# Optimization experiments

Hardware: AMD Instinct MI355X
Metric: run time of the kernel (lower is better)

The kernel has to match this reference:

```python
import jax, jax.numpy as jnp
import numpy as np

DIM = 2048
N_HEADS = 16
HEAD_DIM = 128
EPS = 1e-6


def setup_inputs() -> dict:
    key = jax.random.key(0)
    ks = jax.random.split(key, 8)
    b, gf, gh, gw = 1, 8, 16, 24
    s = gf * gh * gw
    c = HEAD_DIM // 2
    w = lambda k: 0.02 * jax.random.normal(k, (DIM, DIM), jnp.float32)
    return {
        "x": jax.random.normal(ks[0], (b, s, DIM), jnp.float32),
        "freqs_angle": jax.random.normal(ks[1], (1024, c), jnp.float32),
        "Wq": w(ks[2]), "bq": jnp.zeros((DIM,), jnp.float32),
        "Wk": w(ks[3]), "bk": jnp.zeros((DIM,), jnp.float32),
        "Wv": w(ks[4]), "bv": jnp.zeros((DIM,), jnp.float32),
        "Wo": w(ks[5]), "bo": jnp.zeros((DIM,), jnp.float32),
        "gq": jnp.ones((DIM,), jnp.float32),
        "gk": jnp.ones((DIM,), jnp.float32),
        "seq_len": s, "grid_f": gf, "grid_h": gh, "grid_w": gw,
    }


def _rms(t, g):
    return t * jax.lax.rsqrt(jnp.mean(t * t, axis=-1, keepdims=True) + EPS) * g


def _grid_angles(freqs_angle, gf, gh, gw, c):
    # band split [c - 2*(c//3), c//3, c//3] as in rope_apply
    cf = c - 2 * (c // 3)
    ch = cw = c // 3
    af = freqs_angle[:gf, :cf]            # [F, cf]
    ah = freqs_angle[:gh, cf:cf + ch]     # [H, ch]
    aw = freqs_angle[:gw, cf + ch:c]      # [W, cw]
    ang = jnp.concatenate([
        jnp.broadcast_to(af[:, None, None, :], (gf, gh, gw, cf)),
        jnp.broadcast_to(ah[None, :, None, :], (gf, gh, gw, ch)),
        jnp.broadcast_to(aw[None, None, :, :], (gf, gh, gw, cw)),
    ], axis=-1)
    return ang.reshape(gf * gh * gw, c)   # [s, c]


def reference(x, freqs_angle, Wq, bq, Wk, bk, Wv, bv, Wo, bo, gq, gk,
              seq_len, grid_f, grid_h, grid_w):
    b, s, _ = x.shape
    n, d = N_HEADS, HEAD_DIM
    c = d // 2
    ang = _grid_angles(freqs_angle, grid_f, grid_h, grid_w, c)
    cos = jnp.cos(ang)[None, :, None, :]  # [1, s, 1, c]
    sin = jnp.sin(ang)[None, :, None, :]

    def rope(t):  # complex multiply on (even, odd) = (real, imag) pairs
        te, to = t[..., 0::2], t[..., 1::2]
        return jnp.stack([te * cos - to * sin, te * sin + to * cos], axis=-1).reshape(t.shape)

    q = _rms(x @ Wq.T + bq, gq).reshape(b, s, n, d)
    k = _rms(x @ Wk.T + bk, gk).reshape(b, s, n, d)
    v = (x @ Wv.T + bv).reshape(b, s, n, d)
    q, k = rope(q), rope(k)

    scale = np.float32(1.0 / np.sqrt(d))
    scores = jnp.einsum('bqnd,bknd->bnqk', q, k) * scale
    p = jax.nn.softmax(scores, axis=-1)
    o = jnp.einsum('bnqk,bknd->bqnd', p, v).reshape(b, s, n * d)
    return o @ Wo.T + bo
```

## Files before the change

### kernel.cpp

```cpp
#include <hip/hip_runtime.h>
#include <stdint.h>
#include <stddef.h>

typedef __bf16 bf16_t;
typedef __bf16 bf16x8 __attribute__((ext_vector_type(8)));
typedef __bf16 bf16x4 __attribute__((ext_vector_type(4)));
typedef __bf16 bf16x2 __attribute__((ext_vector_type(2)));
typedef float  f32x4  __attribute__((ext_vector_type(4)));

#define SEQ   3072
#define DIMD  2048
#define NH    16
#define HD    128
#define QKVN  6144

__device__ __forceinline__ void async16(const bf16_t* g, bf16_t* l) {
  __builtin_amdgcn_global_load_lds((const __attribute__((address_space(1))) uint32_t*)g,
                                   (__attribute__((address_space(3))) uint32_t*)l, 16, 0, 0);
}

__global__ __launch_bounds__(256) void cvt_bf16(const float* __restrict__ in,
                                                bf16_t* __restrict__ out, int n) {
  int idx = (blockIdx.x * 256 + threadIdx.x) * 8;
  if (idx + 7 < n) {
    const float4 a = *(const float4*)(in + idx);
    const float4 b = *(const float4*)(in + idx + 4);
    bf16x8 o;
    o[0] = (bf16_t)a.x; o[1] = (bf16_t)a.y; o[2] = (bf16_t)a.z; o[3] = (bf16_t)a.w;
    o[4] = (bf16_t)b.x; o[5] = (bf16_t)b.y; o[6] = (bf16_t)b.z; o[7] = (bf16_t)b.w;
    *(bf16x8*)(out + idx) = o;
  }
}

__global__ __launch_bounds__(256) void pack_bias(const float* __restrict__ bq,
                                                 const float* __restrict__ bk,
                                                 const float* __restrict__ bv,
                                                 float* __restrict__ bqkv) {
  int t = blockIdx.x * 256 + threadIdx.x;
  float v;
  if (t < 2048)      v = bq[t];
  else if (t < 4096) v = bk[t - 2048];
  else               v = bv[t - 4096];
  bqkv[t] = v;
}

template<bool OUT_BF16>
__global__ __launch_bounds__(256, 2) void gemm_nt(const bf16_t* __restrict__ A,
                                                  const bf16_t* __restrict__ B,
                                                  const float* __restrict__ bias,
                                                  void* __restrict__ Cout,
                                                  int M, int N, int K) {
  __shared__ __align__(16) bf16_t As[128 * 64];
  __shared__ __align__(16) bf16_t Bs[128 * 64];
  const int t = threadIdx.x;
  const int lane = t & 63, wave = t >> 6;
  const int quad = lane >> 4, l15 = lane & 15;
  const int wy = wave >> 1, wx = wave & 1;
  const size_t bm = (size_t)blockIdx.y * 128, bn = (size_t)blockIdx.x * 128;
  const bf16_t* Ab = A + bm * K;
  const bf16_t* Bb = B + bn * K;
  f32x4 acc[4][4] = {};
  int srow[4], scol[4];
#pragma unroll
  for (int r = 0; r < 4; r++) {
    int L = r * 256 + t;
    int row = L >> 3, cp = L & 7;
    srow[r] = row;
    scol[r] = (cp ^ (row & 7)) * 8;
  }
  for (int k0 = 0; k0 < K; k0 += 64) {
    __syncthreads();
#pragma unroll
    for (int r = 0; r < 4; r++)
      async16(Ab + (size_t)srow[r] * K + k0 + scol[r], &As[(r * 256 + t) * 8]);
#pragma unroll
    for (int r = 0; r < 4; r++)
      async16(Bb + (size_t)srow[r] * K + k0 + scol[r], &Bs[(r * 256 + t) * 8]);
    __syncthreads();
#pragma unroll
    for (int ks = 0; ks < 2; ks++) {
      bf16x8 af[4], bfv[4];
#pragma unroll
      for (int i = 0; i < 4; i++) {
        int row = wy * 64 + i * 16 + l15;
        af[i] = *(const bf16x8*)&As[row * 64 + (((ks * 4 + quad) ^ (row & 7)) * 8)];
      }
#pragma unroll
      for (int j = 0; j < 4; j++) {
        int row = wx * 64 + j * 16 + l15;
        bfv[j] = *(const bf16x8*)&Bs[row * 64 + (((ks * 4 + quad) ^ (row & 7)) * 8)];
      }
#pragma unroll
      for (int i = 0; i < 4; i++)
#pragma unroll
        for (int j = 0; j < 4; j++)
          acc[i][j] = __builtin_amdgcn_mfma_f32_16x16x32_bf16(af[i], bfv[j], acc[i][j], 0, 0, 0);
    }
  }
#pragma unroll
  for (int i = 0; i < 4; i++) {
#pragma unroll
    for (int j = 0; j < 4; j++) {
      size_t row = bm + wy * 64 + i * 16 + quad * 4;
      size_t col = bn + wx * 64 + j * 16 + l15;
      float bb = bias[col];
#pragma unroll
      for (int r = 0; r < 4; r++) {
        float v = acc[i][j][r] + bb;
        if (OUT_BF16) ((bf16_t*)Cout)[(row + r) * N + col] = (bf16_t)v;
        else          ((float*)Cout)[(row + r) * N + col] = v;
      }
    }
  }
}

__global__ __launch_bounds__(256) void rmsrope(bf16_t* __restrict__ qkv,
                                               const float* __restrict__ gq,
                                               const float* __restrict__ gk,
                                               const float* __restrict__ freqs) {
  const int s = blockIdx.x, t = threadIdx.x;
  bf16_t* row = qkv + (size_t)s * QKVN;
  bf16x8 qv = *(const bf16x8*)&row[t * 8];
  bf16x8 kv = *(const bf16x8*)&row[2048 + t * 8];
  float qf[8], kf[8];
  float qs = 0.f, ks2 = 0.f;
#pragma unroll
  for (int i = 0; i < 8; i++) {
    qf[i] = (float)qv[i]; qs  += qf[i] * qf[i];
    kf[i] = (float)kv[i]; ks2 += kf[i] * kf[i];
  }
#pragma unroll
  for (int m = 1; m < 64; m <<= 1) {
    qs  += __shfl_xor(qs, m);
    ks2 += __shfl_xor(ks2, m);
  }
  __shared__ float red[2][4];
  const int wave = t >> 6, lane = t & 63;
  if (lane == 0) { red[0][wave] = qs; red[1][wave] = ks2; }
  __syncthreads();
  qs  = red[0][0] + red[0][1] + red[0][2] + red[0][3];
  ks2 = red[1][0] + red[1][1] + red[1][2] + red[1][3];
  const float qsc = rsqrtf(qs  / 2048.f + 1e-6f);
  const float ksc = rsqrtf(ks2 / 2048.f + 1e-6f);
  const int sf = s / 384, rem = s - sf * 384;
  const int sh = rem / 24, sw = rem - sh * 24;
  bf16x8 qo, ko;
#pragma unroll
  for (int u = 0; u < 4; u++) {
    const int col = t * 8 + 2 * u;
    const int i = (col >> 1) & 63;
    const int frow = (i < 22) ? sf : ((i < 43) ? sh : sw);
    const float ang = freqs[frow * 64 + i];
    float sn, cs;
    __sincosf(ang, &sn, &cs);
    float te = qf[2 * u]     * qsc * gq[col];
    float to = qf[2 * u + 1] * qsc * gq[col + 1];
    qo[2 * u]     = (bf16_t)(te * cs - to * sn);
    qo[2 * u + 1] = (bf16_t)(te * sn + to * cs);
    te = kf[2 * u]     * ksc * gk[col];
    to = kf[2 * u + 1] * ksc * gk[col + 1];
    ko[2 * u]     = (bf16_t)(te * cs - to * sn);
    ko[2 * u + 1] = (bf16_t)(te * sn + to * cs);
  }
  *(bf16x8*)&row[t * 8] = qo;
  *(bf16x8*)&row[2048 + t * 8] = ko;
}

__global__ __launch_bounds__(256, 2) void flash_attn(const bf16_t* __restrict__ qkv,
                                                     bf16_t* __restrict__ ob) {
  __shared__ __align__(16) bf16_t Ks[64 * 128];
  __shared__ __align__(16) bf16_t Vt[128 * 64];
  __shared__ __align__(16) bf16_t Ps[4][32 * 64];
  const int h = blockIdx.y, qt = blockIdx.x;
  const int s0 = qt * 128;
  const int t = threadIdx.x, wave = t >> 6, lane = t & 63;
  const int quad = lane >> 4, l15 = lane & 15;
  const int wq = wave * 32;
  const float scale = 0.08838834764831845f;
  bf16x8 qfr[2][4];
#pragma unroll
  for (int tj = 0; tj < 2; tj++)
#pragma unroll
    for (int ks = 0; ks < 4; ks++)
      qfr[tj][ks] = *(const bf16x8*)&qkv[(size_t)(s0 + wq + tj * 16 + l15) * QKVN + h * HD + ks * 32 + quad * 8];
  f32x4 oacc[2][8] = {};
  float m_run[2] = {-3e38f, -3e38f}, l_run[2] = {0.f, 0.f};
  const int pp = t & 31, bb = t >> 5;
  for (int kt = 0; kt < SEQ / 64; kt++) {
    const int kv0 = kt * 64;
    __syncthreads();
#pragma unroll
    for (int r = 0; r < 4; r++) {
      int L = r * 256 + t, krow = L >> 4, cp = L & 15;
      int c = cp ^ (krow & 7);
      async16(qkv + (size_t)(kv0 + krow) * QKVN + 2048 + h * HD + c * 8, &Ks[L * 8]);
    }
#pragma unroll
    for (int s2 = 0; s2 < 2; s2++) {
      const int d0 = (bb + s2 * 8) * 8;
      bf16x8 va = *(const bf16x8*)&qkv[(size_t)(kv0 + 2 * pp)     * QKVN + 4096 + h * HD + d0];
      bf16x8 vb = *(const bf16x8*)&qkv[(size_t)(kv0 + 2 * pp + 1) * QKVN + 4096 + h * HD + d0];
#pragma unroll
      for (int i = 0; i < 8; i++) {
        const int d = d0 + i;
        const int cp2 = (pp >> 2) ^ (d & 7);
        bf16x2 pr; pr[0] = va[i]; pr[1] = vb[i];
        *(bf16x2*)&Vt[d * 64 + cp2 * 8 + (pp & 3) * 2] = pr;
      }
    }
    __syncthreads();
    f32x4 st[4][2] = {};
#pragma unroll
    for (int ks = 0; ks < 4; ks++) {
      bf16x8 kfr[4];
#pragma unroll
      for (int ti = 0; ti < 4; ti++) {
        const int kr = ti * 16 + l15;
        kfr[ti] = *(const bf16x8*)&Ks[kr * 128 + (((ks * 4 + quad) ^ (kr & 7)) * 8)];
      }
#pragma unroll
      for (int ti = 0; ti < 4; ti++)
#pragma unroll
        for (int tj = 0; tj < 2; tj++)
          st[ti][tj] = __builtin_amdgcn_mfma_f32_16x16x32_bf16(kfr[ti], qfr[tj][ks], st[ti][tj], 0, 0, 0);
    }
    float mt[2] = {-3e38f, -3e38f};
#pragma unroll
    for (int ti = 0; ti < 4; ti++)
#pragma unroll
      for (int tj = 0; tj < 2; tj++)
#pragma unroll
        for (int r = 0; r < 4; r++) {
          st[ti][tj][r] *= scale;
          mt[tj] = fmaxf(mt[tj], st[ti][tj][r]);
        }
    float al[2];
#pragma unroll
    for (int tj = 0; tj < 2; tj++) {
      mt[tj] = fmaxf(mt[tj], __shfl_xor(mt[tj], 16));
      mt[tj] = fmaxf(mt[tj], __shfl_xor(mt[tj], 32));
      const float mn = fmaxf(m_run[tj], mt[tj]);
      al[tj] = __expf(m_run[tj] - mn);
      m_run[tj] = mn;
    }
    float lt[2] = {0.f, 0.f};
#pragma unroll
    for (int ti = 0; ti < 4; ti++)
#pragma unroll
      for (int tj = 0; tj < 2; tj++) {
        bf16x4 pv;
#pragma unroll
        for (int r = 0; r < 4; r++) {
          const float p = __expf(st[ti][tj][r] - m_run[tj]);
          pv[r] = (bf16_t)p;
          lt[tj] += (float)pv[r];
        }
        const int q = tj * 16 + l15;
        const int cp2 = (ti * 2 + (quad >> 1)) ^ (q & 7);
        *(bf16x4*)&Ps[wave][q * 64 + cp2 * 8 + (quad & 1) * 4] = pv;
      }
#pragma unroll
    for (int tj = 0; tj < 2; tj++) {
      lt[tj] += __shfl_xor(lt[tj], 16);
      lt[tj] += __shfl_xor(lt[tj], 32);
      l_run[tj] = l_run[tj] * al[tj] + lt[tj];
    }
#pragma unroll
    for (int ti = 0; ti < 2; ti++) {
      float a0 = __shfl(al[ti], quad * 4 + 0);
      float a1 = __shfl(al[ti], quad * 4 + 1);
      float a2 = __shfl(al[ti], quad * 4 + 2);
      float a3 = __shfl(al[ti], quad * 4 + 3);
#pragma unroll
      for (int dj = 0; dj < 8; dj++) {
        oacc[ti][dj][0] *= a0; oacc[ti][dj][1] *= a1;
        oacc[ti][dj][2] *= a2; oacc[ti][dj][3] *= a3;
      }
    }
#pragma unroll
    for (int ks = 0; ks < 2; ks++) {
      bf16x8 pf[2], vf[8];
#pragma unroll
      for (int ti = 0; ti < 2; ti++) {
        const int q = ti * 16 + l15;
        pf[ti] = *(const bf16x8*)&Ps[wave][q * 64 + (((ks * 4 + quad) ^ (q & 7)) * 8)];
      }
#pragma unroll
      for (int dj = 0; dj < 8; dj++) {
        const int d = dj * 16 + l15;
        vf[dj] = *(const bf16x8*)&Vt[d * 64 + (((ks * 4 + quad) ^ (d & 7)) * 8)];
      }
#pragma unroll
      for (int ti = 0; ti < 2; ti++)
#pragma unroll
        for (int dj = 0; dj < 8; dj++)
          oacc[ti][dj] = __builtin_amdgcn_mfma_f32_16x16x32_bf16(pf[ti], vf[dj], oacc[ti][dj], 0, 0, 0);
    }
  }
#pragma unroll
  for (int ti = 0; ti < 2; ti++) {
    float li[4];
#pragma unroll
    for (int r = 0; r < 4; r++) li[r] = 1.f / __shfl(l_run[ti], quad * 4 + r);
#pragma unroll
    for (int dj = 0; dj < 8; dj++)
#pragma unroll
      for (int r = 0; r < 4; r++) {
        const float v = oacc[ti][dj][r] * li[r];
        ob[(size_t)(s0 + wq + ti * 16 + quad * 4 + r) * DIMD + h * HD + dj * 16 + l15] = (bf16_t)v;
      }
  }
}

extern "C" void kernel_launch(void* const* d_in, const int* in_sizes, int n_in,
                              void* d_out, int out_size, void* d_ws, size_t ws_size,
                              hipStream_t stream) {
  (void)in_sizes; (void)n_in; (void)out_size;
  const float* x     = (const float*)d_in[0];
  const float* freqs = (const float*)d_in[1];
  const float* Wq    = (const float*)d_in[2];
  const float* bq    = (const float*)d_in[3];
  const float* Wk    = (const float*)d_in[4];
  const float* bk    = (const float*)d_in[5];
  const float* Wv    = (const float*)d_in[6];
  const float* bv    = (const float*)d_in[7];
  const float* Wo    = (const float*)d_in[8];
  const float* bo    = (const float*)d_in[9];
  const float* gq    = (const float*)d_in[10];
  const float* gk    = (const float*)d_in[11];

  char* w = (char*)d_ws;
  bf16_t* xb    = (bf16_t*)(w);
  bf16_t* Wqkvb = (bf16_t*)(w + 12582912);
  bf16_t* Wob   = (bf16_t*)(w + 37748736);
  bf16_t* qkvb  = (bf16_t*)(w + 46137344);
  bf16_t* obuf  = (bf16_t*)(w + 83886080);
  float*  bqkv  = (float*) (w + 96468992);
  if (ws_size < (size_t)96493568) return;

  cvt_bf16<<<3072, 256, 0, stream>>>(x, xb, 6291456);
  cvt_bf16<<<2048, 256, 0, stream>>>(Wq, Wqkvb, 4194304);
  cvt_bf16<<<2048, 256, 0, stream>>>(Wk, Wqkvb + 4194304, 4194304);
  cvt_bf16<<<2048, 256, 0, stream>>>(Wv, Wqkvb + 8388608, 4194304);
  cvt_bf16<<<2048, 256, 0, stream>>>(Wo, Wob, 4194304);
  pack_bias<<<24, 256, 0, stream>>>(bq, bk, bv, bqkv);

  gemm_nt<true><<<dim3(48, 24), 256, 0, stream>>>(xb, Wqkvb, bqkv, qkvb, SEQ, QKVN, DIMD);
  rmsrope<<<3072, 256, 0, stream>>>(qkvb, gq, gk, freqs);
  flash_attn<<<dim3(24, NH), 256, 0, stream>>>(qkvb, obuf);
  gemm_nt<false><<<dim3(16, 24), 256, 0, stream>>>(obuf, Wob, bo, (float*)d_out, SEQ, DIMD, DIMD);
}
```

Baseline: 472.5 us.

## Split flash attention KV range in halves and merge with log-sum-exp combine

Flash attention now splits the key/value sequence into two halves along a third grid dimension, doubling the block count from 384 to 768 so more of the GPU's compute units are busy. Each half writes a normalized bf16 partial output plus its running max and sum, and a new combine kernel merges them using softmax rescaling. The launch bound is raised to three blocks per CU. In exchange it adds an extra kernel launch, extra global traffic for the partial outputs, and a second bf16 rounding step. The workspace regions holding the converted x and weights are reused for the partials after the QKV GEMM.

After: 544.0 us. +15.1%, slower.

```diff
diff --git a/kernel.cpp b/kernel.cpp
--- a/kernel.cpp
+++ b/kernel.cpp
@@ -166,12 +166,13 @@
   *(bf16x8*)&row[2048 + t * 8] = ko;
 }
 
-__global__ __launch_bounds__(256, 2) void flash_attn(const bf16_t* __restrict__ qkv,
-                                                     bf16_t* __restrict__ ob) {
+__global__ __launch_bounds__(256, 3) void flash_attn(const bf16_t* __restrict__ qkv,
+                                                     bf16_t* __restrict__ opart,
+                                                     float2* __restrict__ ml) {
   __shared__ __align__(16) bf16_t Ks[64 * 128];
   __shared__ __align__(16) bf16_t Vt[128 * 64];
   __shared__ __align__(16) bf16_t Ps[4][32 * 64];
-  const int h = blockIdx.y, qt = blockIdx.x;
+  const int h = blockIdx.y, qt = blockIdx.x, half = blockIdx.z;
   const int s0 = qt * 128;
   const int t = threadIdx.x, wave = t >> 6, lane = t & 63;
   const int quad = lane >> 4, l15 = lane & 15;
@@ -186,8 +187,8 @@
   f32x4 oacc[2][8] = {};
   float m_run[2] = {-3e38f, -3e38f}, l_run[2] = {0.f, 0.f};
   const int pp = t & 31, bb = t >> 5;
-  for (int kt = 0; kt < SEQ / 64; kt++) {
-    const int kv0 = kt * 64;
+  for (int kt = 0; kt < 24; kt++) {
+    const int kv0 = (half * 24 + kt) * 64;
     __syncthreads();
 #pragma unroll
     for (int r = 0; r < 4; r++) {
@@ -299,6 +300,9 @@
   }
 #pragma unroll
   for (int ti = 0; ti < 2; ti++) {
+    if (quad == 0)
+      ml[(size_t)half * (SEQ * NH) + (size_t)(s0 + wq + ti * 16 + l15) * NH + h] =
+          make_float2(m_run[ti], l_run[ti]);
     float li[4];
 #pragma unroll
     for (int r = 0; r < 4; r++) li[r] = 1.f / __shfl(l_run[ti], quad * 4 + r);
@@ -307,9 +311,30 @@
 #pragma unroll
       for (int r = 0; r < 4; r++) {
         const float v = oacc[ti][dj][r] * li[r];
-        ob[(size_t)(s0 + wq + ti * 16 + quad * 4 + r) * DIMD + h * HD + dj * 16 + l15] = (bf16_t)v;
-      }
-  }
+        opart[(size_t)half * (SEQ * DIMD) +
+              (size_t)(s0 + wq + ti * 16 + quad * 4 + r) * DIMD + h * HD + dj * 16 + l15] = (bf16_t)v;
+      }
+  }
+}
+
+__global__ __launch_bounds__(256) void combine_halves(const bf16_t* __restrict__ opart,
+                                                      const float2* __restrict__ ml,
+                                                      bf16_t* __restrict__ ob) {
+  const int s = blockIdx.x, t = threadIdx.x;
+  const int h = t >> 4;
+  const float2 a = ml[(size_t)s * NH + h];
+  const float2 b = ml[(size_t)(SEQ * NH) + (size_t)s * NH + h];
+  const float mstar = fmaxf(a.x, b.x);
+  float w0 = __expf(a.x - mstar) * a.y;
+  float w1 = __expf(b.x - mstar) * b.y;
+  const float inv = 1.f / (w0 + w1);
+  w0 *= inv; w1 *= inv;
+  const bf16x8 o0 = *(const bf16x8*)&opart[(size_t)s * DIMD + t * 8];
+  const bf16x8 o1 = *(const bf16x8*)&opart[(size_t)(SEQ + s) * DIMD + t * 8];
+  bf16x8 o;
+#pragma unroll
+  for (int i = 0; i < 8; i++) o[i] = (bf16_t)(w0 * (float)o0[i] + w1 * (float)o1[i]);
+  *(bf16x8*)&ob[(size_t)s * DIMD + t * 8] = o;
 }
 
 extern "C" void kernel_launch(void* const* d_in, const int* in_sizes, int n_in,
@@ -336,6 +361,8 @@
   bf16_t* qkvb  = (bf16_t*)(w + 46137344);
   bf16_t* obuf  = (bf16_t*)(w + 83886080);
   float*  bqkv  = (float*) (w + 96468992);
+  bf16_t* opart = (bf16_t*)(w);
+  float2* mlbuf = (float2*)(w + 25165824);
   if (ws_size < (size_t)96493568) return;
 
   cvt_bf16<<<3072, 256, 0, stream>>>(x, xb, 6291456);
@@ -347,6 +374,7 @@
 
   gemm_nt<true><<<dim3(48, 24), 256, 0, stream>>>(xb, Wqkvb, bqkv, qkvb, SEQ, QKVN, DIMD);
   rmsrope<<<3072, 256, 0, stream>>>(qkvb, gq, gk, freqs);
-  flash_attn<<<dim3(24, NH), 256, 0, stream>>>(qkvb, obuf);
+  flash_attn<<<dim3(24, NH, 2), 256, 0, stream>>>(qkvb, opart, mlbuf);
+  combine_halves<<<SEQ, 256, 0, stream>>>(opart, mlbuf, obuf);
   gemm_nt<false><<<dim3(16, 24), 256, 0, stream>>>(obuf, Wob, bo, (float*)d_out, SEQ, DIMD, DIMD);
 }
```
